# Kernel tuning notes

Measured on AMD Instinct MI355X. Metric: run time of the kernel, lower is better.

The kernel has to match this reference:

```python
import jax, jax.numpy as jnp
import numpy as np

# Static cluster layout: B graphs, PER atoms each; first NIN are 'inside'
# (aux_ind==0), remaining NOUT are 'outside' periodic images (aux_ind==1).
B, PER, NIN, K = 256, 1024, 256, 32
NOUT = PER - NIN
N = B * PER
R = 6.0        # cutoff radius (Angstrom)
BOX = 32.0     # box side -> ~30 neighbors within R at this density


def setup_inputs() -> dict:
    key = jax.random.key(0)
    pos = jax.random.uniform(key, (N, 3), dtype=jnp.float32) * BOX
    batch = (jnp.arange(N, dtype=jnp.int32) // PER)
    aux_ind = ((jnp.arange(N, dtype=jnp.int32) % PER) >= NIN).astype(jnp.int32)
    return {"pos": pos, "batch": batch, "aux_ind": aux_ind}


def _select_neighbors(d, valid, k):
    """Pick up to k valid candidates per target, lowest candidate index first.
    d: [..., C] distances, valid: [..., C] bool. Returns (idx, mask, dist),
    each [..., k]; padded slots have mask=False and dist=0."""
    C = d.shape[-1]
    order_key = jnp.where(valid, jnp.arange(C, dtype=jnp.int32), C + 1)
    idx = jnp.argsort(order_key, axis=-1)[..., :k]          # [..., k]
    mask = jnp.take_along_axis(valid, idx, axis=-1)
    dist = jnp.where(mask, jnp.take_along_axis(d, idx, axis=-1), 0.0)
    return idx.astype(jnp.int32), mask, dist


def reference(pos, batch, aux_ind):
    # batch/aux_ind are encoded by the static contiguous layout above;
    # they parameterize the same structure torch builds via scatter_add/cumsum.
    pg = pos.reshape(B, PER, 3)
    ins = pg[:, :NIN]            # [B, NIN, 3]  inside (target + intra-conv) nodes
    outs = pg[:, NIN:]           # [B, NOUT, 3] outside (inter-conv) nodes

    # intra edges: inside -> inside, same graph, no self loops
    d_ii = jnp.sqrt(jnp.sum((ins[:, :, None, :] - ins[:, None, :, :]) ** 2, -1))  # [B,NIN,NIN]
    valid_ii = (d_ii < R) & ~jnp.eye(NIN, dtype=bool)
    idx_ii, m_ii, dist_ii = _select_neighbors(d_ii, valid_ii, K)

    # inter edges: outside -> inside, same graph
    d_io = jnp.sqrt(jnp.sum((ins[:, :, None, :] - outs[:, None, :, :]) ** 2, -1))  # [B,NIN,NOUT]
    valid_io = d_io < R
    idx_io, m_io, dist_io = _select_neighbors(d_io, valid_io, K)

    # relabel to global node indices (flow='source_to_target': row=source, col=target)
    goff = (jnp.arange(B, dtype=jnp.int32) * PER)[:, None, None]       # [B,1,1]
    tgt = jnp.broadcast_to(goff + jnp.arange(NIN, dtype=jnp.int32)[None, :, None],
                           (B, NIN, K))
    src_ii = goff + idx_ii
    src_io = goff + NIN + idx_io

    edge_index = jnp.stack([src_ii.reshape(-1), tgt.reshape(-1)], 0)        # [2, B*NIN*K]
    edge_index_inter = jnp.stack([src_io.reshape(-1), tgt.reshape(-1)], 0)  # [2, B*NIN*K]

    return (edge_index, m_ii.reshape(-1), dist_ii,
            edge_index_inter, m_io.reshape(-1), dist_io)
```

## Files before the change

kernel.cpp:

```cpp
#include <hip/hip_runtime.h>


constexpr int BB    = 256;
constexpr int PERN  = 1024;
constexpr int KK    = 32;
constexpr unsigned EE = 256u * 256u * 32u;

typedef float v2f __attribute__((ext_vector_type(2)));

__device__ __forceinline__ v2f pk_add(v2f a, v2f b) {
    v2f d; asm("v_pk_add_f32 %0, %1, %2" : "=v"(d) : "v"(a), "v"(b)); return d;
}
__device__ __forceinline__ v2f pk_mul(v2f a, v2f b) {
    v2f d; asm("v_pk_mul_f32 %0, %1, %2" : "=v"(d) : "v"(a), "v"(b)); return d;
}

__device__ __forceinline__ int prefix_lt(unsigned long long m) {
    return __builtin_amdgcn_mbcnt_hi((unsigned)(m >> 32),
           __builtin_amdgcn_mbcnt_lo((unsigned)m, 0u));
}

__global__ __launch_bounds__(1024) void mo3e_kernel(const float* __restrict__ pos,
                                                    float* __restrict__ out) {
    __shared__ float sq[3 * PERN];
    __shared__ int   slotbuf[16][64];

    const int b   = blockIdx.x >> 4;
    const int tid = threadIdx.x;
    const int w   = tid >> 6;
    const int l   = tid & 63;
    const int i   = __builtin_amdgcn_readfirstlane((blockIdx.x & 15) * 16 + w);

    {
        const float* gp = pos + (size_t)b * PERN * 3;
        const int fo = (((tid >> 7) << 6) | (tid & 63)) * 2 + ((tid >> 6) & 1);
        sq[fo]            = gp[tid * 3 + 0];
        sq[PERN + fo]     = gp[tid * 3 + 1];
        sq[2 * PERN + fo] = gp[tid * 3 + 2];
    }
    __syncthreads();

    const int fi = (((i >> 7) << 6) | (i & 63)) * 2 + ((i >> 6) & 1);
    const float xi = sq[fi], yi = sq[PERN + fi], zi = sq[2 * PERN + fi];
    const v2f nx = {-xi, -xi}, ny = {-yi, -yi}, nz = {-zi, -zi};

    const v2f* xq = (const v2f*)sq;
    const v2f* yq = (const v2f*)(sq + PERN);
    const v2f* zq = (const v2f*)(sq + 2 * PERN);

    v2f d2v[8];
    {
        v2f cx = xq[l], cy = yq[l], cz = zq[l];
#pragma unroll
        for (int p = 0; p < 8; ++p) {
            v2f tx = cx, ty = cy, tz = cz;
            if (p < 7) {
                tx = xq[(p + 1) * 64 + l];
                ty = yq[(p + 1) * 64 + l];
                tz = zq[(p + 1) * 64 + l];
            }
            const v2f dx = pk_add(cx, nx), dy = pk_add(cy, ny), dz = pk_add(cz, nz);
            d2v[p] = pk_add(pk_add(pk_mul(dx, dx), pk_mul(dy, dy)), pk_mul(dz, dz));
            cx = tx; cy = ty; cz = tz;
        }
    }

    const int  gi       = i >> 6;
    const bool not_self = (l != (i & 63));
    bool va[16];
    unsigned long long msk[16];
#pragma unroll
    for (int g = 0; g < 16; ++g) {
        const int p = g >> 1;
        const float d2 = (g & 1) ? d2v[p].y : d2v[p].x;
        bool v = d2 < 36.0f;
        if (g < 4 && g == gi) v = v && not_self;
        va[g]  = v;
        msk[g] = __ballot(v);
    }

    int* slots = slotbuf[w];

    int S0ii;
    {
        int cnt = 0;
#pragma unroll
        for (int g = 0; g < 4; ++g) {
            const int slot = cnt + prefix_lt(msk[g]);
            if (va[g] && slot < KK) slots[slot] = g * 64 + l;
            cnt += __popcll(msk[g]);
        }
        S0ii = cnt < KK ? cnt : KK;
        if (S0ii < KK) {
            int pc = S0ii;
#pragma unroll
            for (int g = 0; g < 4; ++g) {
                const unsigned long long inv = ~msk[g];
                const int slot = pc + prefix_lt(inv);
                if (!va[g] && slot < KK) slots[slot] = g * 64 + l;
                pc += __popcll(inv);
                if (pc >= KK) break;
            }
        }
    }

    int S0io;
    {
        int cnt = 0;
#pragma unroll
        for (int g = 4; g < 16; ++g) {
            const int slot = cnt + prefix_lt(msk[g]);
            if (va[g] && slot < KK) slots[KK + slot] = g * 64 + l;
            cnt += __popcll(msk[g]);
        }
        S0io = cnt < KK ? cnt : KK;
        if (S0io < KK) {
            int pc = S0io;
#pragma unroll
            for (int g = 4; g < 16; ++g) {
                const unsigned long long inv = ~msk[g];
                const int slot = pc + prefix_lt(inv);
                if (!va[g] && slot < KK) slots[KK + slot] = g * 64 + l;
                pc += __popcll(inv);
                if (pc >= KK) break;
            }
        }
    }

    {
        const int h = l >> 5;
        const int k = l & 31;
        const int idx = slots[l];
        const int fg = (((idx >> 7) << 6) | (idx & 63)) * 2 + ((idx >> 6) & 1);
        const float dxe = xi - sq[fg];
        const float dye = yi - sq[PERN + fg];
        const float dze = zi - sq[2 * PERN + fg];
        const float d2e = dxe * dxe + dye * dye + dze * dze;

        const int S0 = h ? S0io : S0ii;
        const bool mv = k < S0;
        const float dist = mv ? __builtin_amdgcn_sqrtf(d2e) : 0.0f;

        const int goff = b * PERN;
        const unsigned e0  = (unsigned)(b * 256 + i) * KK;
        const unsigned off = (h ? 4u * EE : 0u) + e0 + (unsigned)k;

        out[off]           = (float)(goff + idx);
        out[off + EE]      = (float)(goff + i);
        out[off + 2u * EE] = mv ? 1.0f : 0.0f;
        out[off + 3u * EE] = dist;
    }
}

extern "C" void kernel_launch(void* const* d_in, const int* in_sizes, int n_in,
                              void* d_out, int out_size, void* d_ws, size_t ws_size,
                              hipStream_t stream) {
    const float* pos = (const float*)d_in[0];
    float* out = (float*)d_out;

    mo3e_kernel<<<dim3(BB * 16), dim3(1024), 0, stream>>>(pos, out);
}
```

Baseline: 102.3 us.

## Process four targets per wave with 256-thread blocks and direct scattered stores

Each wave now handles four target atoms instead of one, reusing each shared-memory candidate load across four distance computations, and blocks shrink to 256 threads so each block stages the graph once for 16 targets. Selected neighbor indices and distances are written straight to global memory as they are found, with no per-wave slot buffer. Padding and mask outputs are filled in afterwards. Position staging uses vectorized float4 loads. The risk is more register pressure and scattered, less coalesced stores.

```diff
diff --git a/kernel.cpp b/kernel.cpp
--- a/kernel.cpp
+++ b/kernel.cpp
@@ -1,10 +1,8 @@
 #include <hip/hip_runtime.h>
 
 
-constexpr int BB    = 256;
-constexpr int PERN  = 1024;
-constexpr int KK    = 32;
-constexpr unsigned EE = 256u * 256u * 32u;
+constexpr int KK = 32;
+constexpr unsigned EE = 2097152u;
 
 typedef float v2f __attribute__((ext_vector_type(2)));
 
@@ -20,135 +18,122 @@
            __builtin_amdgcn_mbcnt_lo((unsigned)m, 0u));
 }
 
-__global__ __launch_bounds__(1024) void mo3e_kernel(const float* __restrict__ pos,
-                                                    float* __restrict__ out) {
-    __shared__ float sq[3 * PERN];
-    __shared__ int   slotbuf[16][64];
+__device__ __forceinline__ int fo_of(int j) {
+    return ((((j >> 7) << 6) | (j & 63)) << 1) | ((j >> 6) & 1);
+}
 
-    const int b   = blockIdx.x >> 4;
+__global__ __launch_bounds__(256) void mo3e_kernel(const float* __restrict__ pos,
+                                                   float* __restrict__ out) {
+    __shared__ v2f sqx[512], sqy[512], sqz[512];
+
+    const int blk = blockIdx.x;
+    const int b   = blk >> 4;
     const int tid = threadIdx.x;
     const int w   = tid >> 6;
     const int l   = tid & 63;
-    const int i   = __builtin_amdgcn_readfirstlane((blockIdx.x & 15) * 16 + w);
+    const int t0 = __builtin_amdgcn_readfirstlane(((blk & 15) << 4) | (w << 2));
 
     {
-        const float* gp = pos + (size_t)b * PERN * 3;
-        const int fo = (((tid >> 7) << 6) | (tid & 63)) * 2 + ((tid >> 6) & 1);
-        sq[fo]            = gp[tid * 3 + 0];
-        sq[PERN + fo]     = gp[tid * 3 + 1];
-        sq[2 * PERN + fo] = gp[tid * 3 + 2];
+        const float4* g4 = (const float4*)(pos + (size_t)b * 3072);
+        const float4 A = g4[3 * tid], Bq = g4[3 * tid + 1], C = g4[3 * tid + 2];
+        float* fx = (float*)sqx; float* fy = (float*)sqy; float* fz = (float*)sqz;
+        const float px[4] = {A.x, A.w, Bq.z, C.y};
+        const float py[4] = {A.y, Bq.x, Bq.w, C.z};
+        const float pz[4] = {A.z, Bq.y, C.x, C.w};
+#pragma unroll
+        for (int u = 0; u < 4; ++u) {
+            const int fo = fo_of(4 * tid + u);
+            fx[fo] = px[u]; fy[fo] = py[u]; fz[fo] = pz[u];
+        }
     }
     __syncthreads();
 
-    const int fi = (((i >> 7) << 6) | (i & 63)) * 2 + ((i >> 6) & 1);
-    const float xi = sq[fi], yi = sq[PERN + fi], zi = sq[2 * PERN + fi];
-    const v2f nx = {-xi, -xi}, ny = {-yi, -yi}, nz = {-zi, -zi};
-
-    const v2f* xq = (const v2f*)sq;
-    const v2f* yq = (const v2f*)(sq + PERN);
-    const v2f* zq = (const v2f*)(sq + 2 * PERN);
-
-    v2f d2v[8];
-    {
-        v2f cx = xq[l], cy = yq[l], cz = zq[l];
+    const int goff = b << 10;
+    v2f nx[4], ny[4], nz[4];
+    int gself[4];
+    unsigned e0[4];
+    int cii[4] = {0, 0, 0, 0}, cio[4] = {0, 0, 0, 0};
+    unsigned long long mii[4][4];
 #pragma unroll
-        for (int p = 0; p < 8; ++p) {
-            v2f tx = cx, ty = cy, tz = cz;
-            if (p < 7) {
-                tx = xq[(p + 1) * 64 + l];
-                ty = yq[(p + 1) * 64 + l];
-                tz = zq[(p + 1) * 64 + l];
-            }
-            const v2f dx = pk_add(cx, nx), dy = pk_add(cy, ny), dz = pk_add(cz, nz);
-            d2v[p] = pk_add(pk_add(pk_mul(dx, dx), pk_mul(dy, dy)), pk_mul(dz, dz));
-            cx = tx; cy = ty; cz = tz;
-        }
+    for (int t = 0; t < 4; ++t) {
+        const int it = t0 + t;
+        const int fo = fo_of(it);
+        const float x = ((float*)sqx)[fo], y = ((float*)sqy)[fo], z = ((float*)sqz)[fo];
+        nx[t] = (v2f){-x, -x}; ny[t] = (v2f){-y, -y}; nz[t] = (v2f){-z, -z};
+        gself[t] = it >> 6;
+        e0[t] = (unsigned)((b << 8) + it) << 5;
     }
 
-    const int  gi       = i >> 6;
-    const bool not_self = (l != (i & 63));
-    bool va[16];
-    unsigned long long msk[16];
 #pragma unroll
-    for (int g = 0; g < 16; ++g) {
-        const int p = g >> 1;
-        const float d2 = (g & 1) ? d2v[p].y : d2v[p].x;
-        bool v = d2 < 36.0f;
-        if (g < 4 && g == gi) v = v && not_self;
-        va[g]  = v;
-        msk[g] = __ballot(v);
-    }
-
-    int* slots = slotbuf[w];
-
-    int S0ii;
-    {
-        int cnt = 0;
+    for (int p = 0; p < 8; ++p) {
+        const v2f qx = sqx[(p << 6) + l], qy = sqy[(p << 6) + l], qz = sqz[(p << 6) + l];
 #pragma unroll
-        for (int g = 0; g < 4; ++g) {
-            const int slot = cnt + prefix_lt(msk[g]);
-            if (va[g] && slot < KK) slots[slot] = g * 64 + l;
-            cnt += __popcll(msk[g]);
-        }
-        S0ii = cnt < KK ? cnt : KK;
-        if (S0ii < KK) {
-            int pc = S0ii;
+        for (int t = 0; t < 4; ++t) {
+            const v2f dx = pk_add(qx, nx[t]), dy = pk_add(qy, ny[t]), dz = pk_add(qz, nz[t]);
+            const v2f d2 = pk_add(pk_add(pk_mul(dx, dx), pk_mul(dy, dy)), pk_mul(dz, dz));
 #pragma unroll
-            for (int g = 0; g < 4; ++g) {
-                const unsigned long long inv = ~msk[g];
-                const int slot = pc + prefix_lt(inv);
-                if (!va[g] && slot < KK) slots[slot] = g * 64 + l;
-                pc += __popcll(inv);
-                if (pc >= KK) break;
+            for (int h = 0; h < 2; ++h) {
+                const int g = 2 * p + h;
+                const float d2h = h ? d2.y : d2.x;
+                unsigned long long ms = __ballot(d2h < 36.0f);
+                if (g < 4 && g == gself[t]) ms &= ~(1ull << ((t0 + t) & 63));
+                const int cnt = (g < 4) ? cii[t] : cio[t];
+                const int slot = cnt + prefix_lt(ms);
+                if (((ms >> l) & 1ull) && slot < KK) {
+                    const unsigned base = e0[t] + (g < 4 ? 0u : 4u * EE);
+                    out[base + slot]           = (float)(goff + (g << 6) + l);
+                    out[base + slot + 3u * EE] = __builtin_amdgcn_sqrtf(d2h);
+                }
+                const int ncnt = cnt + (int)__popcll(ms);
+                if (g < 4) { cii[t] = ncnt; mii[t][g] = ms; } else cio[t] = ncnt;
             }
         }
     }
 
-    int S0io;
-    {
-        int cnt = 0;
 #pragma unroll
-        for (int g = 4; g < 16; ++g) {
-            const int slot = cnt + prefix_lt(msk[g]);
-            if (va[g] && slot < KK) slots[KK + slot] = g * 64 + l;
-            cnt += __popcll(msk[g]);
+    for (int t = 0; t < 4; ++t) {
+        const int it = t0 + t;
+        const int S0a = cii[t] < KK ? cii[t] : KK;
+        const int S0b = cio[t] < KK ? cio[t] : KK;
+        const float tv = (float)(goff + it);
+        if (l < KK) {
+            out[e0[t] + l + EE]      = tv;
+            out[e0[t] + l + 5u * EE] = tv;
+            out[e0[t] + l + 2u * EE] = (l < S0a) ? 1.0f : 0.0f;
+            out[e0[t] + l + 6u * EE] = (l < S0b) ? 1.0f : 0.0f;
+            if (l >= S0a) out[e0[t] + l + 3u * EE] = 0.0f;
+            if (l >= S0b) out[e0[t] + l + 7u * EE] = 0.0f;
         }
-        S0io = cnt < KK ? cnt : KK;
-        if (S0io < KK) {
-            int pc = S0io;
+        if (S0a < KK) {
+            int pc = S0a;
 #pragma unroll
-            for (int g = 4; g < 16; ++g) {
-                const unsigned long long inv = ~msk[g];
+            for (int g = 0; g < 4; ++g) {
+                const unsigned long long inv = ~mii[t][g];
                 const int slot = pc + prefix_lt(inv);
-                if (!va[g] && slot < KK) slots[KK + slot] = g * 64 + l;
-                pc += __popcll(inv);
+                if (((inv >> l) & 1ull) && slot < KK)
+                    out[e0[t] + slot] = (float)(goff + (g << 6) + l);
+                pc += (int)__popcll(inv);
                 if (pc >= KK) break;
             }
         }
-    }
-
-    {
-        const int h = l >> 5;
-        const int k = l & 31;
-        const int idx = slots[l];
-        const int fg = (((idx >> 7) << 6) | (idx & 63)) * 2 + ((idx >> 6) & 1);
-        const float dxe = xi - sq[fg];
-        const float dye = yi - sq[PERN + fg];
-        const float dze = zi - sq[2 * PERN + fg];
-        const float d2e = dxe * dxe + dye * dye + dze * dze;
-
-        const int S0 = h ? S0io : S0ii;
-        const bool mv = k < S0;
-        const float dist = mv ? __builtin_amdgcn_sqrtf(d2e) : 0.0f;
-
-        const int goff = b * PERN;
-        const unsigned e0  = (unsigned)(b * 256 + i) * KK;
-        const unsigned off = (h ? 4u * EE : 0u) + e0 + (unsigned)k;
-
-        out[off]           = (float)(goff + idx);
-        out[off + EE]      = (float)(goff + i);
-        out[off + 2u * EE] = mv ? 1.0f : 0.0f;
-        out[off + 3u * EE] = dist;
+        if (S0b < KK) {
+            int pc = S0b;
+            for (int p = 2; p < 8; ++p) {
+                const v2f qx = sqx[(p << 6) + l], qy = sqy[(p << 6) + l], qz = sqz[(p << 6) + l];
+                const v2f dx = pk_add(qx, nx[t]), dy = pk_add(qy, ny[t]), dz = pk_add(qz, nz[t]);
+                const v2f d2 = pk_add(pk_add(pk_mul(dx, dx), pk_mul(dy, dy)), pk_mul(dz, dz));
+#pragma unroll
+                for (int h = 0; h < 2; ++h) {
+                    const float d2h = h ? d2.y : d2.x;
+                    const unsigned long long inv = ~__ballot(d2h < 36.0f);
+                    const int slot = pc + prefix_lt(inv);
+                    if (((inv >> l) & 1ull) && slot < KK)
+                        out[e0[t] + 4u * EE + slot] = (float)(goff + (p << 7) + (h << 6) + l);
+                    pc += (int)__popcll(inv);
+                }
+                if (pc >= KK) break;
+            }
+        }
     }
 }
 
@@ -158,5 +143,5 @@
     const float* pos = (const float*)d_in[0];
     float* out = (float*)d_out;
 
-    mo3e_kernel<<<dim3(BB * 16), dim3(1024), 0, stream>>>(pos, out);
+    mo3e_kernel<<<dim3(4096), dim3(256), 0, stream>>>(pos, out);
 }
```

Result: slower. 115.0 us (+12.4%).
